# Kernel tuning notes

Hardware: AMD Instinct MI355X
Metric: run time of the kernel (lower is better)

## Reference

```python
import jax, jax.numpy as jnp
import numpy as np

B, C, H, W = 8, 64, 64, 64
T, G, HID = 8, 8, 64


def setup_inputs() -> dict:
    key = jax.random.key(0)
    ks = jax.random.split(key, 8)
    s = 0.05
    return {
        "h": jax.random.normal(ks[0], (B, C, H, W), jnp.float32),
        "w_in": jax.random.normal(ks[1], (G * T, C), jnp.float32) * s,
        "b_in": jnp.zeros((G * T,), jnp.float32),
        "w_ih": jax.random.normal(ks[2], (4 * HID, 1), jnp.float32) * s,
        "w_hh": jax.random.normal(ks[3], (4 * HID, HID), jnp.float32) * s,
        "b_ih": jnp.zeros((4 * HID,), jnp.float32),
        "b_hh": jnp.zeros((4 * HID,), jnp.float32),
        "w_s": jax.random.normal(ks[4], (1, HID), jnp.float32) * s,
        "b_s": jnp.zeros((1,), jnp.float32),
        "w_out": jax.random.normal(ks[5], (C, G * T), jnp.float32) * s,
        "b_out": jnp.zeros((C,), jnp.float32),
    }


def reference(h, w_in, b_in, w_ih, w_hh, b_ih, b_hh, w_s, b_s, w_out, b_out):
    Bb, Cc, Hh, Ww = h.shape
    # 1x1 conv in-projection: (B,C,H,W) -> (B,G*T,H,W)
    y = jnp.einsum('bchw,oc->bohw', h, w_in) + b_in[None, :, None, None]
    y = y.reshape(Bb, G, T, Hh, Ww)
    # (B,G,H,W,T) -> (N,T) scalar sequences
    seq = jnp.transpose(y, (0, 1, 3, 4, 2)).reshape(-1, T)
    N = seq.shape[0]
    xs = seq.T  # (T, N) time-major for scan
    bias = b_ih + b_hh  # (4H,)
    w_x = w_ih[:, 0]    # (4H,) scalar-input weights

    def step(carry, x_t):
        hprev, cprev = carry
        # gates: i, f, g, o in torch LSTM ordering
        gates = x_t[:, None] * w_x[None, :] + hprev @ w_hh.T + bias  # (N,4H)
        i, f, g, o = jnp.split(gates, 4, axis=1)
        i = jax.nn.sigmoid(i)
        f = jax.nn.sigmoid(f)
        o = jax.nn.sigmoid(o)
        g = jnp.tanh(g)
        c = f * cprev + i * g
        hn = o * jnp.tanh(c)
        s_t = hn @ w_s[0] + b_s[0]  # fused to_scalar: (N,)
        return (hn, c), s_t

    init = (jnp.zeros((N, HID), h.dtype), jnp.zeros((N, HID), h.dtype))
    _, s = jax.lax.scan(step, init, xs)  # s: (T, N)

    out = s.T.reshape(Bb, G, Hh, Ww, T)
    out = jnp.transpose(out, (0, 1, 4, 2, 3)).reshape(Bb, G * T, Hh, Ww)
    # 1x1 conv out-projection back to C channels
    out = jnp.einsum('bchw,oc->bohw', out, w_out) + b_out[None, :, None, None]
    return out
```

## Files before the change

kernel.cpp:

```cpp
#include <hip/hip_runtime.h>
#include <hip/hip_bf16.h>

#define HW    4096
#define BB    8
#define TT    8

constexpr int OFF_WFRAG = 0;
constexpr int OFF_WTOUT = OFF_WFRAG + 8704;
constexpr int OFF_WXB   = OFF_WTOUT + 4096;

typedef _Float16 halfx8 __attribute__((ext_vector_type(8)));
typedef float    floatx4 __attribute__((ext_vector_type(4)));
typedef float    floatx2 __attribute__((ext_vector_type(2)));

__device__ inline float fast_exp2(float x) {
#if __has_builtin(__builtin_amdgcn_exp2f)
    return __builtin_amdgcn_exp2f(x);
#else
    return __builtin_exp2f(x);
#endif
}
__device__ inline float fast_rcp(float x) {
#if __has_builtin(__builtin_amdgcn_rcpf)
    return __builtin_amdgcn_rcpf(x);
#else
    return 1.0f / x;
#endif
}
__device__ inline floatx2 exp2x2(floatx2 x) {
    floatx2 r; r.x = fast_exp2(x.x); r.y = fast_exp2(x.y); return r;
}
__device__ inline floatx2 rcpx2(floatx2 x) {
    floatx2 r; r.x = fast_rcp(x.x); r.y = fast_rcp(x.y); return r;
}
__device__ inline floatx2 fsig2(floatx2 x) {
    return rcpx2(exp2x2(x * -1.44269504088896f) + 1.0f);
}
__device__ inline floatx2 ftanh2(floatx2 x) {
    floatx2 r = rcpx2(exp2x2(x * 2.88539008177793f) + 1.0f);
    return r * -2.0f + 1.0f;
}

union pack8 { _Float16 h[8]; uint4 u; };

__global__ __launch_bounds__(256) void prep_kernel(
    const float* __restrict__ w_ih,  const float* __restrict__ w_hh,
    const float* __restrict__ b_ih,  const float* __restrict__ b_hh,
    const float* __restrict__ w_s,   const float* __restrict__ w_out,
    float* __restrict__ ws_f) {
    int tid = threadIdx.x;
    if (blockIdx.x == 0) {
        uint4* wf = (uint4*)(ws_f + OFF_WFRAG);
        #pragma unroll
        for (int i = 0; i < 8; ++i) {
            int e  = tid + 256 * i;
            int l  = e & 63;
            int fi = e >> 6;
            int nb = fi >> 1, kc = fi & 1;
            int gate = (l & 15) + 16 * nb;
            int hid  = kc * 32 + (l >> 4) * 8;
            const float* src = w_hh + gate * 64 + hid;
            pack8 p;
            #pragma unroll
            for (int j = 0; j < 8; ++j) p.h[j] = (_Float16)src[j];
            wf[e] = p.u;
        }
        if (tid < 128) {
            int l = tid & 63, kc = tid >> 6;
            pack8 p;
            #pragma unroll
            for (int j = 0; j < 8; ++j) p.h[j] = (_Float16)0.0f;
            if ((l & 15) == 0) {
                #pragma unroll
                for (int j = 0; j < 8; ++j)
                    p.h[j] = (_Float16)w_s[kc * 32 + (l >> 4) * 8 + j];
            }
            wf[2048 + kc * 64 + l] = p.u;
        }
    } else {
        #pragma unroll
        for (int i = 0; i < 16; ++i) {
            int idx = tid + 256 * i;
            int o = idx & 63, c = idx >> 6;
            ws_f[OFF_WTOUT + idx] = w_out[o * 64 + c];
        }
        floatx2* wxb = (floatx2*)(ws_f + OFF_WXB);
        floatx2 v; v.x = w_ih[tid]; v.y = b_ih[tid] + b_hh[tid];
        wxb[tid] = v;
    }
}

__global__ __launch_bounds__(512) void lstm_kernel(
    const float* __restrict__ hin,
    const float* __restrict__ ws_f,
    float* __restrict__ out,
    const float* __restrict__ w_in,
    const float* __restrict__ b_in,
    const float* __restrict__ b_s_p,
    const float* __restrict__ b_out) {
    __shared__ uint4 wfrag_lds[2176];
    __shared__ floatx2 wxb_lds[256];
    __shared__ __align__(16) float x_lds[1024];
    __shared__ __align__(16) _Float16 h_lds[9216];
    __shared__ __align__(16) float stile[1024];
    __shared__ __align__(16) float wt_lds[4096];

    int tid = threadIdx.x;
    int ptile = blockIdx.x & 255;
    int b     = blockIdx.x >> 8;
    int p0 = ptile * 16;

    int lane = tid & 63;
    int wv   = tid >> 6;
    int g    = wv;
    int s    = lane & 15;
    int q    = lane >> 4;

    const uint4* wfg = (const uint4*)(ws_f + OFF_WFRAG);
    #pragma unroll
    for (int i = 0; i < 5; ++i) {
        int e = tid + 512 * i;
        if (e < 2176) wfrag_lds[e] = wfg[e];
    }
    if (tid < 256) wxb_lds[tid] = ((const floatx2*)(ws_f + OFF_WXB))[tid];
    #pragma unroll
    for (int i = 0; i < 2; ++i)
        ((floatx4*)wt_lds)[tid + 512 * i] = ((const floatx4*)w_in)[tid + 512 * i];
    if (tid < 256) {
        int cc = tid >> 2, f4 = tid & 3;
        ((floatx4*)stile)[tid] = *(const floatx4*)&hin[(b * 64 + cc) * HW + p0 + f4 * 4];
    }
    __syncthreads();

    {
        floatx2 xacc; xacc.x = b_in[g * 8 + q]; xacc.y = b_in[g * 8 + q + 4];
        #pragma unroll 8
        for (int cc = 0; cc < 64; ++cc) {
            float hv = stile[cc * 16 + s];
            floatx2 w;
            w.x = wt_lds[(g * 8 + q) * 64 + cc];
            w.y = wt_lds[(g * 8 + q + 4) * 64 + cc];
            floatx2 h2; h2.x = hv; h2.y = hv;
            xacc = xacc + w * h2;
        }
        x_lds[g * 128 + q * 16 + s]       = xacc.x;
        x_lds[g * 128 + (q + 4) * 16 + s] = xacc.y;
    }
    #pragma unroll
    for (int i = 0; i < 9; ++i)
        ((unsigned*)h_lds)[tid + 512 * i] = 0u;
    __syncthreads();

    #pragma unroll
    for (int i = 0; i < 2; ++i)
        ((floatx4*)wt_lds)[tid + 512 * i] =
            ((const floatx4*)(ws_f + OFF_WTOUT))[tid + 512 * i];

    _Float16* hrow = h_lds + wv * 16 * 72;
    float bs = b_s_p[0];

    float c_st[4][4];
    #pragma unroll
    for (int hb = 0; hb < 4; ++hb)
        #pragma unroll
        for (int r = 0; r < 4; ++r) c_st[hb][r] = 0.0f;

    for (int t = 0; t < TT; ++t) {
        asm volatile("" ::: "memory");

        halfx8 a0 = *(const halfx8*)(hrow + s * 72 + q * 8);
        halfx8 a1 = *(const halfx8*)(hrow + s * 72 + q * 8 + 32);

        if (t > 0) {
            halfx8 sb0 = *(const halfx8*)&wfrag_lds[32 * 64 + lane];
            halfx8 sb1 = *(const halfx8*)&wfrag_lds[33 * 64 + lane];
            floatx4 sa = {0.f, 0.f, 0.f, 0.f};
            sa = __builtin_amdgcn_mfma_f32_16x16x32_f16(a0, sb0, sa, 0, 0, 0);
            sa = __builtin_amdgcn_mfma_f32_16x16x32_f16(a1, sb1, sa, 0, 0, 0);
            if (s == 0) {
                floatx4 o4 = {sa[0] + bs, sa[1] + bs, sa[2] + bs, sa[3] + bs};
                *(floatx4*)&stile[(g * 8 + (t - 1)) * 16 + q * 4] = o4;
            }
        }

        floatx4 xv = *(const floatx4*)&x_lds[g * 128 + t * 16 + q * 4];
        floatx2 xlo; xlo.x = xv[0]; xlo.y = xv[1];
        floatx2 xhi; xhi.x = xv[2]; xhi.y = xv[3];

        #pragma unroll
        for (int hb = 0; hb < 4; ++hb) {
            floatx4 acc[4];
            #pragma unroll
            for (int gi = 0; gi < 4; ++gi) {
                int nb = hb + 4 * gi;
                floatx2 wb = wxb_lds[s + 16 * nb];
                floatx2 lo = xlo * wb.x + wb.y;
                floatx2 hi = xhi * wb.x + wb.y;
                floatx4 a = {lo.x, lo.y, hi.x, hi.y};
                halfx8 b0 = *(const halfx8*)&wfrag_lds[(nb * 2 + 0) * 64 + lane];
                halfx8 b1 = *(const halfx8*)&wfrag_lds[(nb * 2 + 1) * 64 + lane];
                a = __builtin_amdgcn_mfma_f32_16x16x32_f16(a0, b0, a, 0, 0, 0);
                a = __builtin_amdgcn_mfma_f32_16x16x32_f16(a1, b1, a, 0, 0, 0);
                acc[gi] = a;
            }
            int s16 = s + 16 * hb;
            _Float16* wp = hrow + (q * 4) * 72 + s16;
            #pragma unroll
            for (int p = 0; p < 2; ++p) {
                int r0 = 2 * p;
                floatx2 iv; iv.x = acc[0][r0]; iv.y = acc[0][r0 + 1]; iv = fsig2(iv);
                floatx2 fv; fv.x = acc[1][r0]; fv.y = acc[1][r0 + 1]; fv = fsig2(fv);
                floatx2 gv; gv.x = acc[2][r0]; gv.y = acc[2][r0 + 1]; gv = ftanh2(gv);
                floatx2 ov; ov.x = acc[3][r0]; ov.y = acc[3][r0 + 1]; ov = fsig2(ov);
                floatx2 cp; cp.x = c_st[hb][r0]; cp.y = c_st[hb][r0 + 1];
                floatx2 c = fv * cp + iv * gv;
                c_st[hb][r0] = c.x; c_st[hb][r0 + 1] = c.y;
                floatx2 hn = ov * ftanh2(c);
                wp[(r0 + 0) * 72] = (_Float16)hn.x;
                wp[(r0 + 1) * 72] = (_Float16)hn.y;
            }
        }
    }
    {
        asm volatile("" ::: "memory");
        halfx8 a0 = *(const halfx8*)(hrow + s * 72 + q * 8);
        halfx8 a1 = *(const halfx8*)(hrow + s * 72 + q * 8 + 32);
        halfx8 sb0 = *(const halfx8*)&wfrag_lds[32 * 64 + lane];
        halfx8 sb1 = *(const halfx8*)&wfrag_lds[33 * 64 + lane];
        floatx4 sa = {0.f, 0.f, 0.f, 0.f};
        sa = __builtin_amdgcn_mfma_f32_16x16x32_f16(a0, sb0, sa, 0, 0, 0);
        sa = __builtin_amdgcn_mfma_f32_16x16x32_f16(a1, sb1, sa, 0, 0, 0);
        if (s == 0) {
            floatx4 o4 = {sa[0] + bs, sa[1] + bs, sa[2] + bs, sa[3] + bs};
            *(floatx4*)&stile[(g * 8 + 7) * 16 + q * 4] = o4;
        }
    }
    __syncthreads();

    {
        int px = tid & 15;
        int oo = tid >> 4;
        floatx2 acc; acc.x = b_out[oo]; acc.y = b_out[oo + 32];
        #pragma unroll 8
        for (int c = 0; c < 64; ++c) {
            float sv = stile[c * 16 + px];
            floatx2 w;
            w.x = wt_lds[c * 64 + oo];
            w.y = wt_lds[c * 64 + oo + 32];
            floatx2 s2; s2.x = sv; s2.y = sv;
            acc = acc + w * s2;
        }
        out[(b * 64 + oo) * HW + p0 + px]      = acc.x;
        out[(b * 64 + oo + 32) * HW + p0 + px] = acc.y;
    }
}

extern "C" void kernel_launch(void* const* d_in, const int* in_sizes, int n_in,
                              void* d_out, int out_size, void* d_ws, size_t ws_size,
                              hipStream_t stream) {
    const float* h     = (const float*)d_in[0];
    const float* w_in  = (const float*)d_in[1];
    const float* b_in  = (const float*)d_in[2];
    const float* w_ih  = (const float*)d_in[3];
    const float* w_hh  = (const float*)d_in[4];
    const float* b_ih  = (const float*)d_in[5];
    const float* b_hh  = (const float*)d_in[6];
    const float* w_s   = (const float*)d_in[7];
    const float* b_s   = (const float*)d_in[8];
    const float* w_out = (const float*)d_in[9];
    const float* b_out = (const float*)d_in[10];
    float* out = (float*)d_out;
    float* ws  = (float*)d_ws;

    prep_kernel<<<2, 256, 0, stream>>>(w_ih, w_hh, b_ih, b_hh, w_s, w_out, ws);
    lstm_kernel<<<2048, 512, 0, stream>>>(h, ws, out, w_in, b_in, b_s, b_out);
}
```

Baseline: 245.3 us.

## Fold exp2 scaling into LSTM weights and merge gate reciprocals algebraically

Pre-scales the recurrent and input weights and biases by -log2(e) (or 2·log2(e) for the g gate) in the prep kernel, so gate pre-activations come out of the MFMA already in exp2 domain. The cell state is kept scaled by 2·log2(e). The gate nonlinearities are rewritten so the cell update and hidden output use two combined reciprocals instead of five separate ones. This removes multiplies and transcendental reciprocals from the serial per-step chain, at the cost of fp16 range and precision changes from the scaled weights and possible overflow in the products of exponentials. The prep kernel is also spread over 12 blocks instead of 2.

```diff
diff --git a/kernel.cpp b/kernel.cpp
--- a/kernel.cpp
+++ b/kernel.cpp
@@ -8,6 +8,9 @@
 constexpr int OFF_WFRAG = 0;
 constexpr int OFF_WTOUT = OFF_WFRAG + 8704;
 constexpr int OFF_WXB   = OFF_WTOUT + 4096;
+
+constexpr float SI = -1.44269504088896340736f;
+constexpr float SG =  2.88539008177792681472f;
 
 typedef _Float16 halfx8 __attribute__((ext_vector_type(8)));
 typedef float    floatx4 __attribute__((ext_vector_type(4)));
@@ -33,13 +36,6 @@
 __device__ inline floatx2 rcpx2(floatx2 x) {
     floatx2 r; r.x = fast_rcp(x.x); r.y = fast_rcp(x.y); return r;
 }
-__device__ inline floatx2 fsig2(floatx2 x) {
-    return rcpx2(exp2x2(x * -1.44269504088896f) + 1.0f);
-}
-__device__ inline floatx2 ftanh2(floatx2 x) {
-    floatx2 r = rcpx2(exp2x2(x * 2.88539008177793f) + 1.0f);
-    return r * -2.0f + 1.0f;
-}
 
 union pack8 { _Float16 h[8]; uint4 u; };
 
@@ -49,24 +45,25 @@
     const float* __restrict__ w_s,   const float* __restrict__ w_out,
     float* __restrict__ ws_f) {
     int tid = threadIdx.x;
-    if (blockIdx.x == 0) {
+    int bid = blockIdx.x;
+    if (bid < 9) {
+        int e = bid * 256 + tid;
         uint4* wf = (uint4*)(ws_f + OFF_WFRAG);
-        #pragma unroll
-        for (int i = 0; i < 8; ++i) {
-            int e  = tid + 256 * i;
+        if (e < 2048) {
             int l  = e & 63;
             int fi = e >> 6;
             int nb = fi >> 1, kc = fi & 1;
             int gate = (l & 15) + 16 * nb;
             int hid  = kc * 32 + (l >> 4) * 8;
+            float sc = (gate >= 128 && gate < 192) ? SG : SI;
             const float* src = w_hh + gate * 64 + hid;
             pack8 p;
             #pragma unroll
-            for (int j = 0; j < 8; ++j) p.h[j] = (_Float16)src[j];
+            for (int j = 0; j < 8; ++j) p.h[j] = (_Float16)(src[j] * sc);
             wf[e] = p.u;
-        }
-        if (tid < 128) {
-            int l = tid & 63, kc = tid >> 6;
+        } else if (e < 2176) {
+            int t2 = e - 2048;
+            int l = t2 & 63, kc = t2 >> 6;
             pack8 p;
             #pragma unroll
             for (int j = 0; j < 8; ++j) p.h[j] = (_Float16)0.0f;
@@ -75,18 +72,20 @@
                 for (int j = 0; j < 8; ++j)
                     p.h[j] = (_Float16)w_s[kc * 32 + (l >> 4) * 8 + j];
             }
-            wf[2048 + kc * 64 + l] = p.u;
-        }
+            wf[e] = p.u;
+        }
+    } else if (bid == 9) {
+        floatx2* wxb = (floatx2*)(ws_f + OFF_WXB);
+        float sc = (tid >= 128 && tid < 192) ? SG : SI;
+        floatx2 v; v.x = w_ih[tid] * sc; v.y = (b_ih[tid] + b_hh[tid]) * sc;
+        wxb[tid] = v;
     } else {
         #pragma unroll
-        for (int i = 0; i < 16; ++i) {
-            int idx = tid + 256 * i;
+        for (int i = 0; i < 8; ++i) {
+            int idx = (bid - 10) * 2048 + tid + 256 * i;
             int o = idx & 63, c = idx >> 6;
             ws_f[OFF_WTOUT + idx] = w_out[o * 64 + c];
         }
-        floatx2* wxb = (floatx2*)(ws_f + OFF_WXB);
-        floatx2 v; v.x = w_ih[tid]; v.y = b_ih[tid] + b_hh[tid];
-        wxb[tid] = v;
     }
 }
 
@@ -208,14 +207,18 @@
             #pragma unroll
             for (int p = 0; p < 2; ++p) {
                 int r0 = 2 * p;
-                floatx2 iv; iv.x = acc[0][r0]; iv.y = acc[0][r0 + 1]; iv = fsig2(iv);
-                floatx2 fv; fv.x = acc[1][r0]; fv.y = acc[1][r0 + 1]; fv = fsig2(fv);
-                floatx2 gv; gv.x = acc[2][r0]; gv.y = acc[2][r0 + 1]; gv = ftanh2(gv);
-                floatx2 ov; ov.x = acc[3][r0]; ov.y = acc[3][r0 + 1]; ov = fsig2(ov);
+                floatx2 Ei; Ei.x = fast_exp2(acc[0][r0]); Ei.y = fast_exp2(acc[0][r0 + 1]);
+                floatx2 Ef; Ef.x = fast_exp2(acc[1][r0]); Ef.y = fast_exp2(acc[1][r0 + 1]);
+                floatx2 Eg; Eg.x = fast_exp2(acc[2][r0]); Eg.y = fast_exp2(acc[2][r0 + 1]);
+                floatx2 Eo; Eo.x = fast_exp2(acc[3][r0]); Eo.y = fast_exp2(acc[3][r0 + 1]);
+                floatx2 Bf  = Ef + 1.0f;
+                floatx2 Pig = (Ei + 1.0f) * (Eg + 1.0f);
                 floatx2 cp; cp.x = c_st[hb][r0]; cp.y = c_st[hb][r0 + 1];
-                floatx2 c = fv * cp + iv * gv;
-                c_st[hb][r0] = c.x; c_st[hb][r0 + 1] = c.y;
-                floatx2 hn = ov * ftanh2(c);
+                floatx2 num = cp * Pig + (Eg * SG - SG) * Bf;
+                floatx2 cs  = num * rcpx2(Bf * Pig);
+                c_st[hb][r0] = cs.x; c_st[hb][r0 + 1] = cs.y;
+                floatx2 Ec  = exp2x2(cs);
+                floatx2 hn  = (Ec - 1.0f) * rcpx2((Eo + 1.0f) * (Ec + 1.0f));
                 wp[(r0 + 0) * 72] = (_Float16)hn.x;
                 wp[(r0 + 1) * 72] = (_Float16)hn.y;
             }
@@ -272,6 +275,6 @@
     float* out = (float*)d_out;
     float* ws  = (float*)d_ws;
 
-    prep_kernel<<<2, 256, 0, stream>>>(w_ih, w_hh, b_ih, b_hh, w_s, w_out, ws);
+    prep_kernel<<<12, 256, 0, stream>>>(w_ih, w_hh, b_ih, b_hh, w_s, w_out, ws);
     lstm_kernel<<<2048, 512, 0, stream>>>(h, ws, out, w_in, b_in, b_s, b_out);
 }
```

New measurement: 232.7 us. 1.05x faster.
